# Kernel tuning notes

Measured on AMD Instinct MI355X. Metric: run time of the kernel, lower is better.

The kernel has to match this reference:

```python
import jax, jax.numpy as jnp
import numpy as np

IN, H1, H2, H3, H4, OUT = 512, 2048, 2048, 1024, 512, 1


def setup_inputs() -> dict:
    key = jax.random.key(0)
    ks = jax.random.split(key, 12)
    def lin(k, fan_in, fan_out):
        # torch Linear default init: U(-1/sqrt(fan_in), 1/sqrt(fan_in))
        bound = 1.0 / np.sqrt(fan_in)
        k1, k2 = jax.random.split(k)
        W = jax.random.uniform(k1, (fan_out, fan_in), jnp.float32, -bound, bound)
        b = jax.random.uniform(k2, (fan_out,), jnp.float32, -bound, bound)
        return W, b
    x = jax.random.normal(ks[0], (16384, IN), jnp.float32)
    cross_w = jnp.ones((IN,), jnp.float32)   # init.constant_(1.0)
    cross_b = jnp.zeros((IN,), jnp.float32)  # init.constant_(0.0)
    W1, b1 = lin(ks[1], IN, H1)
    W2, b2 = lin(ks[2], H1, H2)
    W3, b3 = lin(ks[3], H2, H3)
    W4, b4 = lin(ks[4], H3, H4)
    Wo, bo = lin(ks[5], H4, OUT)
    return {"x": x, "cross_w": cross_w, "cross_b": cross_b,
            "W1": W1, "b1": b1, "W2": W2, "b2": b2,
            "W3": W3, "b3": b3, "W4": W4, "b4": b4,
            "Wo": Wo, "bo": bo}


def reference(x, cross_w, cross_b, W1, b1, W2, b2, W3, b3, W4, b4, Wo, bo):
    # Cross layer: bmm(x0[...,None], x[...,None,:]) . w == x0 * (x . w)
    # (mathematically identical, avoids the O(f^2) outer product)
    xw = x @ cross_w                         # [B]
    h = x * xw[:, None] + cross_b + x        # [B, IN]
    h = jax.nn.relu(h @ W1.T + b1)           # [B, H1]
    h = jax.nn.relu(h @ W2.T + b2)           # [B, H2]
    h = jax.nn.relu(h @ W3.T + b3)           # [B, H3]
    h = jax.nn.relu(h @ W4.T + b4)           # [B, H4]
    return h @ Wo.T + bo                     # [B, OUT]
```

## Files before the change

kernel.cpp:

```cpp
#include <hip/hip_runtime.h>


#define BM 128
#define BN 128
#define BK 32

typedef __bf16 bf16x8 __attribute__((ext_vector_type(8)));
typedef float  f32x4  __attribute__((ext_vector_type(4)));
typedef unsigned short u16x4 __attribute__((ext_vector_type(4)));
typedef float  f32x4v __attribute__((ext_vector_type(4)));

__device__ __forceinline__ unsigned short f2bf(float f) {
    unsigned int u = __builtin_bit_cast(unsigned int, f);
    u += 0x7fffu + ((u >> 16) & 1u);
    return (unsigned short)(u >> 16);
}
__device__ __forceinline__ float bf2f(unsigned short h) {
    unsigned int u = ((unsigned int)h) << 16;
    return __builtin_bit_cast(float, u);
}

__device__ __forceinline__ void async16(const void* g, void* l) {
    __builtin_amdgcn_global_load_lds(
        (const __attribute__((address_space(1))) unsigned int*)g,
        (__attribute__((address_space(3))) unsigned int*)l,
        16, 0, 0);
}

__global__ __launch_bounds__(256, 2)
void gemm_bt_bias_relu(const unsigned short* __restrict__ A,
                       const unsigned short* __restrict__ B,
                       const float* __restrict__ bias,
                       unsigned short* __restrict__ C,
                       int M, int N, int K)
{
    __shared__ __align__(16) unsigned short As[BM * BK];
    __shared__ __align__(16) unsigned short Bs[BN * BK];

    const int tid  = threadIdx.x;
    const int lane = tid & 63;
    const int wave = tid >> 6;
    const int quad = lane >> 4;
    const int l16  = lane & 15;

    const int bm = blockIdx.x * BM;
    const int bn = blockIdx.y * BN;
    const int wm = (wave & 1) * 64;
    const int wn = (wave >> 1) * 64;

    const int lrow = tid >> 2;
    const int lcol = (tid & 3) * 8;

    const unsigned short* ga  = A + (size_t)(bm + lrow) * K + lcol;
    const unsigned short* ga2 = ga + (size_t)64 * K;
    const unsigned short* gb  = B + (size_t)(bn + lrow) * K + lcol;
    const unsigned short* gb2 = gb + (size_t)64 * K;

    unsigned short* lA  = As + tid * 8;
    unsigned short* lA2 = lA + 2048;
    unsigned short* lB  = Bs + tid * 8;
    unsigned short* lB2 = lB + 2048;

    const unsigned short* As_w = As + (wm + l16) * BK + quad * 8;
    const unsigned short* Bs_w = Bs + (wn + l16) * BK + quad * 8;

    f32x4 acc[4][4] = {};

    for (int k0 = 0; k0 < K; k0 += BK) {
        async16(ga  + k0, lA);
        async16(ga2 + k0, lA2);
        async16(gb  + k0, lB);
        async16(gb2 + k0, lB2);
        __syncthreads();

        bf16x8 af[4], bfr[4];
#pragma unroll
        for (int i = 0; i < 4; ++i) af[i]  = *(const bf16x8*)(As_w + i * 16 * BK);
#pragma unroll
        for (int j = 0; j < 4; ++j) bfr[j] = *(const bf16x8*)(Bs_w + j * 16 * BK);
#pragma unroll
        for (int i = 0; i < 4; ++i)
#pragma unroll
            for (int j = 0; j < 4; ++j)
                acc[i][j] = __builtin_amdgcn_mfma_f32_16x16x32_bf16(
                    af[i], bfr[j], acc[i][j], 0, 0, 0);
        __syncthreads();
    }

    float bv[4];
#pragma unroll
    for (int j = 0; j < 4; ++j) bv[j] = bias[bn + wn + j * 16 + l16];

#pragma unroll
    for (int i = 0; i < 4; ++i) {
        const int row0 = bm + wm + i * 16 + quad * 4;
#pragma unroll
        for (int j = 0; j < 4; ++j) {
            const int col = bn + wn + j * 16 + l16;
#pragma unroll
            for (int r = 0; r < 4; ++r) {
                float v = acc[i][j][r] + bv[j];
                v = fmaxf(v, 0.0f);
                C[(size_t)(row0 + r) * N + col] = f2bf(v);
            }
        }
    }
}

__global__ __launch_bounds__(256)
void cross_kernel(const float* __restrict__ x, const float* __restrict__ cw,
                  const float* __restrict__ cb, unsigned short* __restrict__ h0)
{
    const int row  = blockIdx.x * 4 + (threadIdx.x >> 6);
    const int lane = threadIdx.x & 63;
    const float* xr = x + (size_t)row * 512;
    float xv[8];
    float s = 0.f;
#pragma unroll
    for (int i = 0; i < 8; ++i) {
        const int c = lane + i * 64;
        xv[i] = xr[c];
        s += xv[i] * cw[c];
    }
#pragma unroll
    for (int off = 32; off > 0; off >>= 1) s += __shfl_down(s, off, 64);
    s = __shfl(s, 0, 64);
    unsigned short* hr = h0 + (size_t)row * 512;
#pragma unroll
    for (int i = 0; i < 8; ++i) {
        const int c = lane + i * 64;
        hr[c] = f2bf(xv[i] * s + cb[c] + xv[i]);
    }
}

__global__ __launch_bounds__(256)
void final_dot(const unsigned short* __restrict__ h4, const float* __restrict__ Wo,
               const float* __restrict__ bo, float* __restrict__ out)
{
    const int row  = blockIdx.x * 4 + (threadIdx.x >> 6);
    const int lane = threadIdx.x & 63;
    const unsigned short* hr = h4 + (size_t)row * 512;
    float s = 0.f;
#pragma unroll
    for (int i = 0; i < 8; ++i) {
        const int c = lane + i * 64;
        s += bf2f(hr[c]) * Wo[c];
    }
#pragma unroll
    for (int off = 32; off > 0; off >>= 1) s += __shfl_down(s, off, 64);
    if (lane == 0) out[row] = s + bo[0];
}

__global__ __launch_bounds__(256)
void convert_weights(const float* __restrict__ s1, const float* __restrict__ s2,
                     const float* __restrict__ s3, const float* __restrict__ s4,
                     unsigned short* __restrict__ d1, unsigned short* __restrict__ d2,
                     unsigned short* __restrict__ d3, unsigned short* __restrict__ d4)
{
    long t = (long)blockIdx.x * 256 + threadIdx.x;
    const float* s; unsigned short* d; long off;
    if (t < 262144L)       { s = s1; d = d1; off = t; }
    else if (t < 1310720L) { s = s2; d = d2; off = t - 262144L; }
    else if (t < 1835008L) { s = s3; d = d3; off = t - 1310720L; }
    else                   { s = s4; d = d4; off = t - 1835008L; }
    f32x4 f = *(const f32x4*)(s + off * 4);
    u16x4 o;
#pragma unroll
    for (int i = 0; i < 4; ++i) o[i] = f2bf(f[i]);
    *(u16x4*)(d + off * 4) = o;
}

extern "C" void kernel_launch(void* const* d_in, const int* in_sizes, int n_in,
                              void* d_out, int out_size, void* d_ws, size_t ws_size,
                              hipStream_t stream)
{
    const float* x  = (const float*)d_in[0];
    const float* cw = (const float*)d_in[1];
    const float* cb = (const float*)d_in[2];
    const float* W1 = (const float*)d_in[3];  const float* b1 = (const float*)d_in[4];
    const float* W2 = (const float*)d_in[5];  const float* b2 = (const float*)d_in[6];
    const float* W3 = (const float*)d_in[7];  const float* b3 = (const float*)d_in[8];
    const float* W4 = (const float*)d_in[9];  const float* b4 = (const float*)d_in[10];
    const float* Wo = (const float*)d_in[11]; const float* bo = (const float*)d_in[12];
    float* out = (float*)d_out;

    char* p = (char*)d_ws;
    unsigned short* wb1 = (unsigned short*)p; p += (size_t)2048 * 512  * 2;
    unsigned short* wb2 = (unsigned short*)p; p += (size_t)2048 * 2048 * 2;
    unsigned short* wb3 = (unsigned short*)p; p += (size_t)1024 * 2048 * 2;
    unsigned short* wb4 = (unsigned short*)p; p += (size_t)512  * 1024 * 2;
    unsigned short* actA = (unsigned short*)p; p += (size_t)16384 * 2048 * 2;
    unsigned short* actB = (unsigned short*)p;

    convert_weights<<<7680, 256, 0, stream>>>(W1, W2, W3, W4, wb1, wb2, wb3, wb4);
    cross_kernel<<<4096, 256, 0, stream>>>(x, cw, cb, actA);

    gemm_bt_bias_relu<<<dim3(128, 16), 256, 0, stream>>>(actA, wb1, b1, actB, 16384, 2048, 512);
    gemm_bt_bias_relu<<<dim3(128, 16), 256, 0, stream>>>(actB, wb2, b2, actA, 16384, 2048, 2048);
    gemm_bt_bias_relu<<<dim3(128, 8), 256, 0, stream>>>(actA, wb3, b3, actB, 16384, 1024, 2048);
    gemm_bt_bias_relu<<<dim3(128, 4), 256, 0, stream>>>(actB, wb4, b4, actA, 16384, 512, 1024);
    final_dot<<<4096, 256, 0, stream>>>(actA, Wo, bo, out);
}
```

Measured before the change: 416.9 us.

## Double GEMM K-tile to 64 and XOR-swizzle LDS layout to avoid bank conflicts

Raises the GEMM K-tile from 32 to 64, so each loop iteration issues 8 async global-to-LDS loads and runs two 16x16x32 MFMA sub-steps, halving the number of barrier pairs per K. The global source column is XOR-swizzled by row so the LDS tile lands in a permuted layout, and the fragment reads apply the same XOR to avoid LDS bank conflicts on the 128-byte row stride. LDS use doubles to 32 KB per block, which could limit occupancy. There is still no double buffering, so load latency remains exposed.

```diff
diff --git a/kernel.cpp b/kernel.cpp
--- a/kernel.cpp
+++ b/kernel.cpp
@@ -3,12 +3,11 @@
 
 #define BM 128
 #define BN 128
-#define BK 32
+#define BK 64
 
 typedef __bf16 bf16x8 __attribute__((ext_vector_type(8)));
 typedef float  f32x4  __attribute__((ext_vector_type(4)));
 typedef unsigned short u16x4 __attribute__((ext_vector_type(4)));
-typedef float  f32x4v __attribute__((ext_vector_type(4)));
 
 __device__ __forceinline__ unsigned short f2bf(float f) {
     unsigned int u = __builtin_bit_cast(unsigned int, f);
@@ -48,42 +47,46 @@
     const int wm = (wave & 1) * 64;
     const int wn = (wave >> 1) * 64;
 
-    const int lrow = tid >> 2;
-    const int lcol = (tid & 3) * 8;
-
-    const unsigned short* ga  = A + (size_t)(bm + lrow) * K + lcol;
-    const unsigned short* ga2 = ga + (size_t)64 * K;
-    const unsigned short* gb  = B + (size_t)(bn + lrow) * K + lcol;
-    const unsigned short* gb2 = gb + (size_t)64 * K;
-
-    unsigned short* lA  = As + tid * 8;
-    unsigned short* lA2 = lA + 2048;
-    unsigned short* lB  = Bs + tid * 8;
-    unsigned short* lB2 = lB + 2048;
-
-    const unsigned short* As_w = As + (wm + l16) * BK + quad * 8;
-    const unsigned short* Bs_w = Bs + (wn + l16) * BK + quad * 8;
+    const int lrow = tid >> 3;
+    const int gcol = ((tid & 7) ^ (lrow & 7)) * 8;
+
+    const unsigned short* gaBase = A + (size_t)(bm + lrow) * K + gcol;
+    const unsigned short* gbBase = B + (size_t)(bn + lrow) * K + gcol;
+
+    unsigned short* lA = As + tid * 8;
+    unsigned short* lB = Bs + tid * 8;
+
+    const int xa = l16 & 7;
+    const unsigned short* As_w = As + (wm + l16) * BK;
+    const unsigned short* Bs_w = Bs + (wn + l16) * BK;
+    const int c0 = (quad ^ xa) * 8;
+    const int c1 = ((quad ^ 4) ^ xa) * 8;
 
     f32x4 acc[4][4] = {};
 
     for (int k0 = 0; k0 < K; k0 += BK) {
-        async16(ga  + k0, lA);
-        async16(ga2 + k0, lA2);
-        async16(gb  + k0, lB);
-        async16(gb2 + k0, lB2);
+#pragma unroll
+        for (int i = 0; i < 4; ++i) {
+            async16(gaBase + (size_t)(i * 32) * K + k0, lA + i * 2048);
+            async16(gbBase + (size_t)(i * 32) * K + k0, lB + i * 2048);
+        }
         __syncthreads();
 
-        bf16x8 af[4], bfr[4];
-#pragma unroll
-        for (int i = 0; i < 4; ++i) af[i]  = *(const bf16x8*)(As_w + i * 16 * BK);
-#pragma unroll
-        for (int j = 0; j < 4; ++j) bfr[j] = *(const bf16x8*)(Bs_w + j * 16 * BK);
-#pragma unroll
-        for (int i = 0; i < 4; ++i)
-#pragma unroll
-            for (int j = 0; j < 4; ++j)
-                acc[i][j] = __builtin_amdgcn_mfma_f32_16x16x32_bf16(
-                    af[i], bfr[j], acc[i][j], 0, 0, 0);
+#pragma unroll
+        for (int kk = 0; kk < 2; ++kk) {
+            const int cs = kk ? c1 : c0;
+            bf16x8 af[4], bfr[4];
+#pragma unroll
+            for (int i = 0; i < 4; ++i) af[i]  = *(const bf16x8*)(As_w + i * 16 * BK + cs);
+#pragma unroll
+            for (int j = 0; j < 4; ++j) bfr[j] = *(const bf16x8*)(Bs_w + j * 16 * BK + cs);
+#pragma unroll
+            for (int i = 0; i < 4; ++i)
+#pragma unroll
+                for (int j = 0; j < 4; ++j)
+                    acc[i][j] = __builtin_amdgcn_mfma_f32_16x16x32_bf16(
+                        af[i], bfr[j], acc[i][j], 0, 0, 0);
+        }
         __syncthreads();
     }
 
```

Result: faster. 380.8 us (-8.7%).
